# Kernel tuning notes

Measured on AMD Instinct MI355X. Metric: run time of the kernel, lower is better.

The kernel has to match this reference:

```python
import jax, jax.numpy as jnp
import numpy as np

EMBEDDING_DIM = 128
METRIC_MARGIN = 1.0
EPS = 1e-8


def setup_inputs() -> dict:
    key = jax.random.key(0)
    X = jax.random.normal(key, (8192, EMBEDDING_DIM), dtype=jnp.float32)
    return {"X": X}


def reference(X):
    B, d = X.shape
    P = B // 2  # number of positive pairs (2p, 2p+1)
    # Pairwise similarity matrix (original uses broadcasted mul+sum; this is the GEMM form)
    D = (X @ X.T) / d  # [B, B]
    E = jnp.exp(D + METRIC_MARGIN)  # [B, B]

    # For pair p: sum of exp over rows 2p and 2p+1, excluding columns {2p, 2p+1}
    pair_row_sum = E.sum(axis=1).reshape(P, 2).sum(axis=1)  # [P]
    # 2x2 diagonal blocks E[2p:2p+2, 2p:2p+2]
    blocks = jnp.einsum('pipj->pij', E.reshape(P, 2, P, 2))  # [P, 2, 2]
    S = pair_row_sum - blocks.sum(axis=(1, 2))  # [P]

    even = jnp.arange(0, B, 2)
    D_pos = D[even, even + 1]  # D[2p, 2p+1], [P]

    J = jnp.log(EPS + S) - D_pos  # [P]
    loss = jnp.mean(jnp.maximum(J, 0.0) ** 2) / 2.0
    return loss
```

## Files before the change

kernel.cpp:

```cpp
#include <hip/hip_runtime.h>
#include <hip/hip_bf16.h>

#define NROWS 8192
#define DIM   128
#define NPAIR (NROWS / 2)
#define CSPLIT 32
#define COLS_PER_CS (NROWS / CSPLIT)
#define NTILES (COLS_PER_CS / 16)
#define MREP 2
#define ROWS_PER_BLOCK 128

typedef __attribute__((ext_vector_type(8))) short bf16x8;
typedef __attribute__((ext_vector_type(4))) float f32x4;

__device__ inline float exp2_fast(float x) {
#if __has_builtin(__builtin_amdgcn_exp2f)
    return __builtin_amdgcn_exp2f(x);
#else
    return exp2f(x);
#endif
}

__device__ inline unsigned short f2bf(float f) {
    unsigned int u = __float_as_uint(f);
    unsigned int r = (u + 0x7fffu + ((u >> 16) & 1u)) >> 16;
    return (unsigned short)r;
}

#define SCL_F 0.0112710550069450f
#define E1_F  2.7182818284590452f

__global__ __launch_bounds__(256) void k_pack(const float* __restrict__ X,
                                              unsigned short* __restrict__ Pa,
                                              unsigned short* __restrict__ Pb) {
    int id = blockIdx.x * 256 + threadIdx.x;
    float4 v = reinterpret_cast<const float4*>(X)[id];
    int r  = id >> 5;
    int k0 = (id & 31) * 4;
    int tile = r >> 4;
    int g    = k0 >> 5;
    int lhi  = (k0 >> 3) & 3;
    int e0   = k0 & 7;
    size_t base = ((size_t)(tile * 4 + g) * 64 + lhi * 16 + (r & 15)) * 8 + e0;
    ushort4 oa, ob;
    oa.x = f2bf(v.x * SCL_F); oa.y = f2bf(v.y * SCL_F);
    oa.z = f2bf(v.z * SCL_F); oa.w = f2bf(v.w * SCL_F);
    ob.x = f2bf(v.x); ob.y = f2bf(v.y); ob.z = f2bf(v.z); ob.w = f2bf(v.w);
    *reinterpret_cast<ushort4*>(Pa + base) = oa;
    *reinterpret_cast<ushort4*>(Pb + base) = ob;
}

#define MFMA16(A, B, D) __builtin_amdgcn_mfma_f32_16x16x32_bf16(A, B, D, 0, 0, 0)

__global__ void k_rowsum(const unsigned short* __restrict__ Pa,
                         const unsigned short* __restrict__ Pb,
                         float* __restrict__ partial) {
    const int wave = threadIdx.x >> 6;
    const int lane = threadIdx.x & 63;
    const int l15  = lane & 15;
    const int lhi  = lane >> 4;
    const int rowbase = blockIdx.x * ROWS_PER_BLOCK + wave * (MREP * 16);
    const int rb0 = rowbase >> 4;
    const int cs  = blockIdx.y;

    const bf16x8* PA = reinterpret_cast<const bf16x8*>(Pa);
    const bf16x8* PB = reinterpret_cast<const bf16x8*>(Pb);

    bf16x8 a00 = PA[(size_t)(rb0 * 4 + 0) * 64 + lane];
    bf16x8 a01 = PA[(size_t)(rb0 * 4 + 1) * 64 + lane];
    bf16x8 a02 = PA[(size_t)(rb0 * 4 + 2) * 64 + lane];
    bf16x8 a03 = PA[(size_t)(rb0 * 4 + 3) * 64 + lane];
    bf16x8 a10 = PA[(size_t)(rb0 * 4 + 4) * 64 + lane];
    bf16x8 a11 = PA[(size_t)(rb0 * 4 + 5) * 64 + lane];
    bf16x8 a12 = PA[(size_t)(rb0 * 4 + 6) * 64 + lane];
    bf16x8 a13 = PA[(size_t)(rb0 * 4 + 7) * 64 + lane];
    asm volatile("" : "+v"(a00), "+v"(a01), "+v"(a02), "+v"(a03));
    asm volatile("" : "+v"(a10), "+v"(a11), "+v"(a12), "+v"(a13));

    f32x4 esum0 = {0.f, 0.f, 0.f, 0.f};
    f32x4 esum1 = {0.f, 0.f, 0.f, 0.f};

    size_t tb = (size_t)cs * NTILES * 256 + lane;

    for (int ct = 0; ct < NTILES; ++ct) {
        bf16x8 b0 = PB[tb];
        bf16x8 b1 = PB[tb + 64];
        bf16x8 b2 = PB[tb + 128];
        bf16x8 b3 = PB[tb + 192];
        tb += 256;

        f32x4 d0 = {0.f, 0.f, 0.f, 0.f};
        f32x4 d1 = {0.f, 0.f, 0.f, 0.f};
        d0 = MFMA16(a00, b0, d0); d1 = MFMA16(a10, b0, d1);
        d0 = MFMA16(a01, b1, d0); d1 = MFMA16(a11, b1, d1);
        d0 = MFMA16(a02, b2, d0); d1 = MFMA16(a12, b2, d1);
        d0 = MFMA16(a03, b3, d0); d1 = MFMA16(a13, b3, d1);

        esum0[0] += exp2_fast(d0[0]); esum0[1] += exp2_fast(d0[1]);
        esum0[2] += exp2_fast(d0[2]); esum0[3] += exp2_fast(d0[3]);
        esum1[0] += exp2_fast(d1[0]); esum1[1] += exp2_fast(d1[1]);
        esum1[2] += exp2_fast(d1[2]); esum1[3] += exp2_fast(d1[3]);
    }

#pragma unroll
    for (int m = 0; m < MREP; ++m) {
#pragma unroll
        for (int j = 0; j < 4; ++j) {
            float v = (m == 0) ? esum0[j] : esum1[j];
            v += __shfl_xor(v, 1, 64);
            v += __shfl_xor(v, 2, 64);
            v += __shfl_xor(v, 4, 64);
            v += __shfl_xor(v, 8, 64);
            if (l15 == 0) {
                int row = rowbase + m * 16 + lhi * 4 + j;
                partial[(size_t)row * CSPLIT + cs] = v * E1_F;
            }
        }
    }
}

__global__ __launch_bounds__(256) void k_loss1(const float* __restrict__ X,
                                               const float* __restrict__ partial,
                                               float* __restrict__ lpart) {
    int p = blockIdx.x * 256 + threadIdx.x;
    const float4* a = reinterpret_cast<const float4*>(X + (size_t)(2 * p) * DIM);
    const float4* b = reinterpret_cast<const float4*>(X + (size_t)(2 * p + 1) * DIM);
    float d00 = 0.f, d01 = 0.f, d11 = 0.f;
#pragma unroll 8
    for (int i = 0; i < DIM / 4; ++i) {
        float4 av = a[i], bv = b[i];
        d00 += av.x * av.x + av.y * av.y + av.z * av.z + av.w * av.w;
        d01 += av.x * bv.x + av.y * bv.y + av.z * bv.z + av.w * bv.w;
        d11 += bv.x * bv.x + bv.y * bv.y + bv.z * bv.z + bv.w * bv.w;
    }
    float D01 = d01 * (1.0f / DIM);
    float blocksum = __expf(d00 * (1.0f / DIM) + 1.0f)
                   + 2.0f * __expf(D01 + 1.0f)
                   + __expf(d11 * (1.0f / DIM) + 1.0f);

    const float4* pp = reinterpret_cast<const float4*>(partial + (size_t)(2 * p) * CSPLIT);
    float S = 0.0f;
#pragma unroll
    for (int i = 0; i < 2 * CSPLIT / 4; ++i) {
        float4 v = pp[i];
        S += v.x + v.y + v.z + v.w;
    }
    S -= blocksum;
    float J = logf(1e-8f + S) - D01;
    float t = fmaxf(J, 0.0f);
    float acc = t * t;

    __shared__ float red[4];
    float v = acc;
#pragma unroll
    for (int off = 32; off >= 1; off >>= 1) v += __shfl_down(v, off, 64);
    if ((threadIdx.x & 63) == 0) red[threadIdx.x >> 6] = v;
    __syncthreads();
    if (threadIdx.x == 0)
        lpart[blockIdx.x] = red[0] + red[1] + red[2] + red[3];
}

__global__ __launch_bounds__(64) void k_final(const float* __restrict__ lpart,
                                              float* __restrict__ out) {
    float v = (threadIdx.x < 16) ? lpart[threadIdx.x] : 0.0f;
#pragma unroll
    for (int off = 8; off >= 1; off >>= 1) v += __shfl_down(v, off, 64);
    if (threadIdx.x == 0) out[0] = v * (1.0f / (2.0f * NPAIR));
}

extern "C" void kernel_launch(void* const* d_in, const int* in_sizes, int n_in,
                              void* d_out, int out_size, void* d_ws, size_t ws_size,
                              hipStream_t stream) {
    const float* X = (const float*)d_in[0];
    float* out = (float*)d_out;

    unsigned short* Pa = (unsigned short*)d_ws;
    unsigned short* Pb = Pa + (size_t)NROWS * DIM;
    float* partial = (float*)(Pb + (size_t)NROWS * DIM);
    float* lpart = partial + (size_t)NROWS * CSPLIT;

    k_pack<<<dim3((NROWS * DIM / 4) / 256), dim3(256), 0, stream>>>(X, Pa, Pb);
    k_rowsum<<<dim3(NROWS / ROWS_PER_BLOCK, CSPLIT), dim3(256), 0, stream>>>(Pa, Pb, partial);
    k_loss1<<<dim3(NPAIR / 256), dim3(256), 0, stream>>>(X, partial, lpart);
    k_final<<<dim3(1), dim3(64), 0, stream>>>(lpart, out);
}
```

Measured before the change: 43.86 us.

## Double row tiles per wave and pin A fragments in AGPRs

Each wave now computes four 16-row tiles instead of two against each loaded B tile, so every B fragment load feeds twice as many MFMAs. The column split is doubled so the grid keeps a similar block count. The A operands are forced into accumulator registers through inline asm constraints, which frees VGPRs but may add copies or a compile issue if MFMA cannot read them directly. More in-flight MFMA chains give more independent work per iteration at the cost of register pressure, and the loss kernel now reads twice as many partial sums per row.

```diff
diff --git a/kernel.cpp b/kernel.cpp
--- a/kernel.cpp
+++ b/kernel.cpp
@@ -4,11 +4,11 @@
 #define NROWS 8192
 #define DIM   128
 #define NPAIR (NROWS / 2)
-#define CSPLIT 32
+#define CSPLIT 64
 #define COLS_PER_CS (NROWS / CSPLIT)
 #define NTILES (COLS_PER_CS / 16)
-#define MREP 2
-#define ROWS_PER_BLOCK 128
+#define MREP 4
+#define ROWS_PER_BLOCK 256
 
 typedef __attribute__((ext_vector_type(8))) short bf16x8;
 typedef __attribute__((ext_vector_type(4))) float f32x4;
@@ -52,9 +52,10 @@
 
 #define MFMA16(A, B, D) __builtin_amdgcn_mfma_f32_16x16x32_bf16(A, B, D, 0, 0, 0)
 
-__global__ void k_rowsum(const unsigned short* __restrict__ Pa,
-                         const unsigned short* __restrict__ Pb,
-                         float* __restrict__ partial) {
+__global__ __launch_bounds__(256)
+void k_rowsum(const unsigned short* __restrict__ Pa,
+              const unsigned short* __restrict__ Pb,
+              float* __restrict__ partial) {
     const int wave = threadIdx.x >> 6;
     const int lane = threadIdx.x & 63;
     const int l15  = lane & 15;
@@ -66,19 +67,29 @@
     const bf16x8* PA = reinterpret_cast<const bf16x8*>(Pa);
     const bf16x8* PB = reinterpret_cast<const bf16x8*>(Pb);
 
-    bf16x8 a00 = PA[(size_t)(rb0 * 4 + 0) * 64 + lane];
-    bf16x8 a01 = PA[(size_t)(rb0 * 4 + 1) * 64 + lane];
-    bf16x8 a02 = PA[(size_t)(rb0 * 4 + 2) * 64 + lane];
-    bf16x8 a03 = PA[(size_t)(rb0 * 4 + 3) * 64 + lane];
-    bf16x8 a10 = PA[(size_t)(rb0 * 4 + 4) * 64 + lane];
-    bf16x8 a11 = PA[(size_t)(rb0 * 4 + 5) * 64 + lane];
-    bf16x8 a12 = PA[(size_t)(rb0 * 4 + 6) * 64 + lane];
-    bf16x8 a13 = PA[(size_t)(rb0 * 4 + 7) * 64 + lane];
-    asm volatile("" : "+v"(a00), "+v"(a01), "+v"(a02), "+v"(a03));
-    asm volatile("" : "+v"(a10), "+v"(a11), "+v"(a12), "+v"(a13));
-
-    f32x4 esum0 = {0.f, 0.f, 0.f, 0.f};
-    f32x4 esum1 = {0.f, 0.f, 0.f, 0.f};
+    bf16x8 a00 = PA[(size_t)(rb0 * 4 +  0) * 64 + lane];
+    bf16x8 a01 = PA[(size_t)(rb0 * 4 +  1) * 64 + lane];
+    bf16x8 a02 = PA[(size_t)(rb0 * 4 +  2) * 64 + lane];
+    bf16x8 a03 = PA[(size_t)(rb0 * 4 +  3) * 64 + lane];
+    bf16x8 a10 = PA[(size_t)(rb0 * 4 +  4) * 64 + lane];
+    bf16x8 a11 = PA[(size_t)(rb0 * 4 +  5) * 64 + lane];
+    bf16x8 a12 = PA[(size_t)(rb0 * 4 +  6) * 64 + lane];
+    bf16x8 a13 = PA[(size_t)(rb0 * 4 +  7) * 64 + lane];
+    bf16x8 a20 = PA[(size_t)(rb0 * 4 +  8) * 64 + lane];
+    bf16x8 a21 = PA[(size_t)(rb0 * 4 +  9) * 64 + lane];
+    bf16x8 a22 = PA[(size_t)(rb0 * 4 + 10) * 64 + lane];
+    bf16x8 a23 = PA[(size_t)(rb0 * 4 + 11) * 64 + lane];
+    bf16x8 a30 = PA[(size_t)(rb0 * 4 + 12) * 64 + lane];
+    bf16x8 a31 = PA[(size_t)(rb0 * 4 + 13) * 64 + lane];
+    bf16x8 a32 = PA[(size_t)(rb0 * 4 + 14) * 64 + lane];
+    bf16x8 a33 = PA[(size_t)(rb0 * 4 + 15) * 64 + lane];
+    asm volatile("" : "+a"(a00), "+a"(a01), "+a"(a02), "+a"(a03));
+    asm volatile("" : "+a"(a10), "+a"(a11), "+a"(a12), "+a"(a13));
+    asm volatile("" : "+a"(a20), "+a"(a21), "+a"(a22), "+a"(a23));
+    asm volatile("" : "+a"(a30), "+a"(a31), "+a"(a32), "+a"(a33));
+
+    f32x4 es0 = {0.f,0.f,0.f,0.f}, es1 = {0.f,0.f,0.f,0.f};
+    f32x4 es2 = {0.f,0.f,0.f,0.f}, es3 = {0.f,0.f,0.f,0.f};
 
     size_t tb = (size_t)cs * NTILES * 256 + lane;
 
@@ -89,24 +100,33 @@
         bf16x8 b3 = PB[tb + 192];
         tb += 256;
 
-        f32x4 d0 = {0.f, 0.f, 0.f, 0.f};
-        f32x4 d1 = {0.f, 0.f, 0.f, 0.f};
+        f32x4 d0 = {0.f,0.f,0.f,0.f}, d1 = {0.f,0.f,0.f,0.f};
+        f32x4 d2 = {0.f,0.f,0.f,0.f}, d3 = {0.f,0.f,0.f,0.f};
         d0 = MFMA16(a00, b0, d0); d1 = MFMA16(a10, b0, d1);
+        d2 = MFMA16(a20, b0, d2); d3 = MFMA16(a30, b0, d3);
         d0 = MFMA16(a01, b1, d0); d1 = MFMA16(a11, b1, d1);
+        d2 = MFMA16(a21, b1, d2); d3 = MFMA16(a31, b1, d3);
         d0 = MFMA16(a02, b2, d0); d1 = MFMA16(a12, b2, d1);
+        d2 = MFMA16(a22, b2, d2); d3 = MFMA16(a32, b2, d3);
         d0 = MFMA16(a03, b3, d0); d1 = MFMA16(a13, b3, d1);
-
-        esum0[0] += exp2_fast(d0[0]); esum0[1] += exp2_fast(d0[1]);
-        esum0[2] += exp2_fast(d0[2]); esum0[3] += exp2_fast(d0[3]);
-        esum1[0] += exp2_fast(d1[0]); esum1[1] += exp2_fast(d1[1]);
-        esum1[2] += exp2_fast(d1[2]); esum1[3] += exp2_fast(d1[3]);
+        d2 = MFMA16(a23, b3, d2); d3 = MFMA16(a33, b3, d3);
+
+        es0[0] += exp2_fast(d0[0]); es0[1] += exp2_fast(d0[1]);
+        es0[2] += exp2_fast(d0[2]); es0[3] += exp2_fast(d0[3]);
+        es1[0] += exp2_fast(d1[0]); es1[1] += exp2_fast(d1[1]);
+        es1[2] += exp2_fast(d1[2]); es1[3] += exp2_fast(d1[3]);
+        es2[0] += exp2_fast(d2[0]); es2[1] += exp2_fast(d2[1]);
+        es2[2] += exp2_fast(d2[2]); es2[3] += exp2_fast(d2[3]);
+        es3[0] += exp2_fast(d3[0]); es3[1] += exp2_fast(d3[1]);
+        es3[2] += exp2_fast(d3[2]); es3[3] += exp2_fast(d3[3]);
     }
 
 #pragma unroll
     for (int m = 0; m < MREP; ++m) {
 #pragma unroll
         for (int j = 0; j < 4; ++j) {
-            float v = (m == 0) ? esum0[j] : esum1[j];
+            float v = (m == 0) ? es0[j] : (m == 1) ? es1[j]
+                    : (m == 2) ? es2[j] : es3[j];
             v += __shfl_xor(v, 1, 64);
             v += __shfl_xor(v, 2, 64);
             v += __shfl_xor(v, 4, 64);
```

New measurement: 47.67 us. 8.7% more time.
